# Performance work log

Hardware: AMD Instinct MI355X
Metric: run time of the kernel (lower is better)

Reference implementation:

```python
import jax, jax.numpy as jnp
import numpy as np


def setup_inputs() -> dict:
    key = jax.random.key(0)
    k1, k2 = jax.random.split(key)
    num_classes, queries_per_class, prototypes_per_class, embedding_dim = 19, 5, 5, 1024
    batch = 1024
    num_queries = num_classes * queries_per_class  # 95
    query_features = jax.random.normal(k1, (batch, num_queries, embedding_dim), dtype=jnp.float32)
    # nn.Embedding default init: N(0,1)
    weight = jax.random.normal(k2, (num_classes * (prototypes_per_class + 1), embedding_dim), dtype=jnp.float32)
    return {
        "query_features": query_features,
        "weight": weight,
        "num_classes": num_classes,
        "queries_per_class": queries_per_class,
        "prototypes_per_class": prototypes_per_class,
    }


def reference(query_features, weight, num_classes, queries_per_class, prototypes_per_class):
    B, Q, D = query_features.shape
    P = prototypes_per_class
    # class index for each query: [Q]
    class_indices = jnp.repeat(jnp.arange(num_classes), queries_per_class)
    # prototype row indices per query: [Q, P+1]
    proto_indices = class_indices[:, None] * (P + 1) + jnp.arange(P + 1)[None, :]
    # gathered prototypes: [Q, P+1, D] (shared across batch; no batch expansion)
    proto = weight[proto_indices]
    # positive sims against the P class prototypes: [B, Q, P]
    pos_sim = jnp.einsum("bqd,qkd->bqk", query_features, proto[:, :P, :])
    # background sim against last embedding: [B, Q]
    bg_sim = jnp.einsum("bqd,qd->bq", query_features, proto[:, P, :])
    pos_max = jnp.max(pos_sim, axis=-1)  # [B, Q]
    logits = jnp.full((B, Q, num_classes + 1), -jnp.inf, dtype=query_features.dtype)
    logits = logits.at[:, jnp.arange(Q), class_indices].set(pos_max)
    logits = logits.at[:, :, -1].set(bg_sim)
    return logits
```

## Files before the change

### kernel.cpp

```cpp
#include <hip/hip_runtime.h>
#include <math.h>
#include <float.h>


#define NB 4
#define NEG_FILL (-3.0e38f)

__global__ __launch_bounds__(256) void codebook_head_kernel(
    const float* __restrict__ qf,
    const float* __restrict__ w,
    float* __restrict__ out,
    int B, int Q, int D,
    int num_classes, int qpc, int P)
{
    const int wave_id = (blockIdx.x * blockDim.x + threadIdx.x) >> 6;
    const int lane    = threadIdx.x & 63;
    const int bblocks = (B + NB - 1) / NB;
    const int total   = bblocks * Q;
    if (wave_id >= total) return;

    const int q   = wave_id % Q;
    const int b0  = (wave_id / Q) * NB;
    const int cls = q / qpc;

    const float* proto = w + (size_t)cls * (P + 1) * D;

    float acc[6][NB];
#pragma unroll
    for (int k = 0; k < 6; ++k)
#pragma unroll
        for (int j = 0; j < NB; ++j)
            acc[k][j] = 0.f;

    for (int d0 = lane * 4; d0 < D; d0 += 64 * 4) {
        float4 pv[6];
#pragma unroll
        for (int k = 0; k < 6; ++k)
            pv[k] = *reinterpret_cast<const float4*>(proto + (size_t)k * D + d0);

#pragma unroll
        for (int j = 0; j < NB; ++j) {
            const int bj = (b0 + j < B) ? (b0 + j) : (B - 1);
            const float4 qv =
                *reinterpret_cast<const float4*>(qf + ((size_t)bj * Q + q) * D + d0);
#pragma unroll
            for (int k = 0; k < 6; ++k)
                acc[k][j] += qv.x * pv[k].x + qv.y * pv[k].y +
                             qv.z * pv[k].z + qv.w * pv[k].w;
        }
    }

#pragma unroll
    for (int k = 0; k < 6; ++k) {
#pragma unroll
        for (int j = 0; j < NB; ++j) {
            float v = acc[k][j];
#pragma unroll
            for (int off = 32; off > 0; off >>= 1)
                v += __shfl_xor(v, off);
            acc[k][j] = v;
        }
    }

#pragma unroll
    for (int j = 0; j < NB; ++j) {
        if (b0 + j >= B) break;
        const float pos_max = fmaxf(fmaxf(fmaxf(acc[0][j], acc[1][j]),
                                          fmaxf(acc[2][j], acc[3][j])), acc[4][j]);
        const float bg = acc[5][j];
        float* orow = out + ((size_t)(b0 + j) * Q + q) * (num_classes + 1);
        if (lane < num_classes + 1) {
            float v = NEG_FILL;
            if (lane == cls)         v = pos_max;
            if (lane == num_classes) v = bg;
            orow[lane] = v;
        }
    }
}

extern "C" void kernel_launch(void* const* d_in, const int* in_sizes, int n_in,
                              void* d_out, int out_size, void* d_ws, size_t ws_size,
                              hipStream_t stream)
{
    const float* qf = (const float*)d_in[0];
    const float* w  = (const float*)d_in[1];
    float* out = (float*)d_out;

    const int num_classes = 19;
    const int qpc         = 5;
    const int P           = 5;
    const int rows        = num_classes * (P + 1);
    const int D           = in_sizes[1] / rows;
    const int Q           = num_classes * qpc;
    const int B           = in_sizes[0] / (Q * D);

    const int bblocks = (B + NB - 1) / NB;
    const int total_waves = bblocks * Q;
    const int waves_per_block = 4;
    const int blocks = (total_waves + waves_per_block - 1) / waves_per_block;

    codebook_head_kernel<<<blocks, waves_per_block * 64, 0, stream>>>(
        qf, w, out, B, Q, D, num_classes, qpc, P);
}
```

Baseline: 92.37 us.

## Use bf16 MFMA 32x32x16 for query-prototype dot products with nontemporal loads

Adds a matrix-core path in which each wave takes 32 batch rows of one query and multiplies them against that query's class prototype rows with bf16 MFMA 32x32x16. Activations and weights are converted from fp32 to bf16 in registers. Query loads are nontemporal, and the max and background reduction goes through shared memory before vectorized f32x4 output stores. This aims to cut the ALU cost of fp32 dot products, but it lowers precision to bf16 and spends 32 MFMA columns where only 6 are useful.

```diff
diff --git a/kernel.cpp b/kernel.cpp
--- a/kernel.cpp
+++ b/kernel.cpp
@@ -3,66 +3,145 @@
 #include <float.h>
 
 
-#define NB 4
+typedef float    f32x4  __attribute__((ext_vector_type(4)));
+typedef float    f32x16 __attribute__((ext_vector_type(16)));
+typedef short    bf16x8 __attribute__((ext_vector_type(8)));
+typedef unsigned u32x4  __attribute__((ext_vector_type(4)));
+
 #define NEG_FILL (-3.0e38f)
 
-__global__ __launch_bounds__(256) void codebook_head_kernel(
+static __device__ __forceinline__ unsigned pack2_bf16(float lo, float hi) {
+    unsigned ul = __builtin_bit_cast(unsigned, lo);
+    unsigned uh = __builtin_bit_cast(unsigned, hi);
+    ul += 0x7FFFu + ((ul >> 16) & 1u);
+    uh += 0x7FFFu + ((uh >> 16) & 1u);
+    return (ul >> 16) | (uh & 0xFFFF0000u);
+}
+
+static __device__ __forceinline__ bf16x8 cvt8(f32x4 a, f32x4 b) {
+    u32x4 u;
+    u.x = pack2_bf16(a.x, a.y);
+    u.y = pack2_bf16(a.z, a.w);
+    u.z = pack2_bf16(b.x, b.y);
+    u.w = pack2_bf16(b.z, b.w);
+    return __builtin_bit_cast(bf16x8, u);
+}
+
+__global__ __launch_bounds__(256) void codebook_head_mfma(
     const float* __restrict__ qf,
     const float* __restrict__ w,
     float* __restrict__ out,
     int B, int Q, int D,
+    int NC, int qpc, int P)
+{
+    const int lane = threadIdx.x & 63;
+    const int wid  = threadIdx.x >> 6;
+
+    const int bt_count = B >> 5;
+    const int total    = bt_count * Q;
+    int wave_id = blockIdx.x * 4 + wid;
+    if (wave_id >= total) wave_id = total - 1;
+
+    const int q   = wave_id % Q;
+    const int bt  = wave_id / Q;
+    const int cls = q / qpc;
+
+    const int col  = lane & 31;
+    const int hi   = lane >> 5;
+    const int koff = hi * 8;
+
+    int arow = bt * 32 + col; if (arow >= B) arow = B - 1;
+    const float* aptr = qf + ((size_t)arow * Q + q) * D + koff;
+
+    const int wrows = NC * (P + 1);
+    int wrow = cls * (P + 1) + col; if (wrow >= wrows) wrow = wrows - 1;
+    const float* bptr = w + (size_t)wrow * D + koff;
+
+    f32x16 acc;
+#pragma unroll
+    for (int i = 0; i < 16; ++i) acc[i] = 0.f;
+
+    const int ntiles = D >> 4;
+#pragma unroll 4
+    for (int kt = 0; kt < ntiles; ++kt) {
+        const int off = kt * 16;
+        const f32x4 a0 = __builtin_nontemporal_load(
+            reinterpret_cast<const f32x4*>(aptr + off));
+        const f32x4 a1 = __builtin_nontemporal_load(
+            reinterpret_cast<const f32x4*>(aptr + off + 4));
+        const f32x4 b0 = *reinterpret_cast<const f32x4*>(bptr + off);
+        const f32x4 b1 = *reinterpret_cast<const f32x4*>(bptr + off + 4);
+        acc = __builtin_amdgcn_mfma_f32_32x32x16_bf16(
+            cvt8(a0, a1), cvt8(b0, b1), acc, 0, 0, 0);
+    }
+
+    __shared__ float red[4][32][2];
+
+#pragma unroll
+    for (int r = 0; r < 16; ++r) {
+        float v = (col < 5) ? acc[r] : -FLT_MAX;
+        v = fmaxf(v, __shfl_xor(v, 1));
+        v = fmaxf(v, __shfl_xor(v, 2));
+        v = fmaxf(v, __shfl_xor(v, 4));
+        const int row = (r & 3) + 8 * (r >> 2) + 4 * hi;
+        if (col == 0) red[wid][row][0] = v;
+        if (col == 5) red[wid][row][1] = acc[r];
+    }
+    __syncthreads();
+
+    const int NCp1 = NC + 1;
+    for (int e = lane; e < 32 * 5; e += 64) {
+        const int r  = e / 5;
+        const int c0 = (e - 5 * r) * 4;
+        const int brow = bt * 32 + r;
+        if (brow >= B) continue;
+        const float pm  = red[wid][r][0];
+        const float bgv = red[wid][r][1];
+        f32x4 v;
+#pragma unroll
+        for (int t = 0; t < 4; ++t) {
+            const int c = c0 + t;
+            float x = NEG_FILL;
+            if (c == cls) x = pm;
+            if (c == NC)  x = bgv;
+            v[t] = x;
+        }
+        *reinterpret_cast<f32x4*>(out + ((size_t)brow * Q + q) * NCp1 + c0) = v;
+    }
+}
+
+#define NB 4
+__global__ __launch_bounds__(256) void codebook_head_kernel_gen(
+    const float* __restrict__ qf, const float* __restrict__ w,
+    float* __restrict__ out, int B, int Q, int D,
     int num_classes, int qpc, int P)
 {
     const int wave_id = (blockIdx.x * blockDim.x + threadIdx.x) >> 6;
     const int lane    = threadIdx.x & 63;
     const int bblocks = (B + NB - 1) / NB;
-    const int total   = bblocks * Q;
-    if (wave_id >= total) return;
-
-    const int q   = wave_id % Q;
-    const int b0  = (wave_id / Q) * NB;
-    const int cls = q / qpc;
-
+    if (wave_id >= bblocks * Q) return;
+    const int q = wave_id % Q, b0 = (wave_id / Q) * NB, cls = q / qpc;
     const float* proto = w + (size_t)cls * (P + 1) * D;
-
     float acc[6][NB];
-#pragma unroll
     for (int k = 0; k < 6; ++k)
-#pragma unroll
-        for (int j = 0; j < NB; ++j)
-            acc[k][j] = 0.f;
-
-    for (int d0 = lane * 4; d0 < D; d0 += 64 * 4) {
-        float4 pv[6];
-#pragma unroll
+        for (int j = 0; j < NB; ++j) acc[k][j] = 0.f;
+    for (int d = lane * 4; d < D; d += 256) {
+        f32x4 pv[6];
         for (int k = 0; k < 6; ++k)
-            pv[k] = *reinterpret_cast<const float4*>(proto + (size_t)k * D + d0);
-
-#pragma unroll
+            pv[k] = *reinterpret_cast<const f32x4*>(proto + (size_t)k * D + d);
         for (int j = 0; j < NB; ++j) {
             const int bj = (b0 + j < B) ? (b0 + j) : (B - 1);
-            const float4 qv =
-                *reinterpret_cast<const float4*>(qf + ((size_t)bj * Q + q) * D + d0);
-#pragma unroll
+            const f32x4 qv = *reinterpret_cast<const f32x4*>(qf + ((size_t)bj * Q + q) * D + d);
             for (int k = 0; k < 6; ++k)
-                acc[k][j] += qv.x * pv[k].x + qv.y * pv[k].y +
-                             qv.z * pv[k].z + qv.w * pv[k].w;
+                acc[k][j] += qv.x * pv[k].x + qv.y * pv[k].y + qv.z * pv[k].z + qv.w * pv[k].w;
         }
     }
-
-#pragma unroll
-    for (int k = 0; k < 6; ++k) {
-#pragma unroll
+    for (int k = 0; k < 6; ++k)
         for (int j = 0; j < NB; ++j) {
             float v = acc[k][j];
-#pragma unroll
-            for (int off = 32; off > 0; off >>= 1)
-                v += __shfl_xor(v, off);
+            for (int off = 32; off > 0; off >>= 1) v += __shfl_xor(v, off);
             acc[k][j] = v;
         }
-    }
-
-#pragma unroll
     for (int j = 0; j < NB; ++j) {
         if (b0 + j >= B) break;
         const float pos_max = fmaxf(fmaxf(fmaxf(acc[0][j], acc[1][j]),
@@ -94,11 +173,16 @@
     const int Q           = num_classes * qpc;
     const int B           = in_sizes[0] / (Q * D);
 
-    const int bblocks = (B + NB - 1) / NB;
-    const int total_waves = bblocks * Q;
-    const int waves_per_block = 4;
-    const int blocks = (total_waves + waves_per_block - 1) / waves_per_block;
-
-    codebook_head_kernel<<<blocks, waves_per_block * 64, 0, stream>>>(
-        qf, w, out, B, Q, D, num_classes, qpc, P);
+    if ((B % 32) == 0 && (D % 16) == 0) {
+        const int total_waves = (B / 32) * Q;
+        const int blocks = (total_waves + 3) / 4;
+        codebook_head_mfma<<<blocks, 256, 0, stream>>>(
+            qf, w, out, B, Q, D, num_classes, qpc, P);
+    } else {
+        const int bblocks = (B + NB - 1) / NB;
+        const int total_waves = bblocks * Q;
+        const int blocks = (total_waves + 3) / 4;
+        codebook_head_kernel_gen<<<blocks, 256, 0, stream>>>(
+            qf, w, out, B, Q, D, num_classes, qpc, P);
+    }
 }
```

After: 203.1 us. +119.9%, slower.
